# Kernel tuning notes

Measured on AMD Instinct MI355X. Metric: run time of the kernel, lower is better.

Reference implementation:

```python
import jax, jax.numpy as jnp
import numpy as np
from jax import lax

# HF MambaConfig defaults with vocab_size=2048, hidden_size=128
V, DM, NL, I, N, K, R = 2048, 128, 32, 256, 16, 4, 8  # vocab, d_model, layers, intermediate, ssm_state, conv_kernel, dt_rank
B, L = 8, 2048
EPS = 1e-5


def _rms(x, w):
    return x * lax.rsqrt(jnp.mean(x * x, axis=-1, keepdims=True) + EPS) * w


def _block(x, p):
    res = x
    h = _rms(x, p['norm_w'])
    hz = h @ p['in_proj_w'].T                            # (B,L,2I)
    hs, gate = hz[..., :I], hz[..., I:]
    # depthwise causal conv over time
    c = lax.conv_general_dilated(hs.transpose(0, 2, 1), p['conv_w'][:, None, :],
                                 (1,), [(K - 1, 0)],
                                 dimension_numbers=('NCH', 'OIH', 'NCH'),
                                 feature_group_count=I)
    hs = jax.nn.silu((c + p['conv_b'][None, :, None]).transpose(0, 2, 1))  # (B,L,I)
    xp = hs @ p['x_proj_w'].T                            # (B,L,R+2N)
    dt, Bm, Cm = xp[..., :R], xp[..., R:R + N], xp[..., R + N:]
    dt = jax.nn.softplus(dt @ p['dt_proj_w'].T + p['dt_proj_b'])           # (B,L,I)
    A = -jnp.exp(p['A_log'])                             # (I,N)
    dA = jnp.exp(dt[..., None] * A)                      # (B,L,I,N)
    dBu = dt[..., None] * Bm[:, :, None, :] * hs[..., None]               # (B,L,I,N)

    # selective scan: h_t = dA_t * h_{t-1} + dBu_t, via parallel associative scan
    def comb(e1, e2):
        a1, b1 = e1
        a2, b2 = e2
        return a2 * a1, a2 * b1 + b2

    _, hstates = lax.associative_scan(comb, (dA, dBu), axis=1)
    y = jnp.einsum('blin,bln->bli', hstates, Cm) + hs * p['D']
    y = y * jax.nn.silu(gate)
    return res + y @ p['out_proj_w'].T


def setup_inputs() -> dict:
    key = jax.random.key(0)
    ks = jax.random.split(key, 10)

    def rn(k, shape, s):
        return jax.random.normal(k, shape, jnp.float32) * s

    a_init = jnp.tile(jnp.log(jnp.arange(1, N + 1, dtype=jnp.float32)), (NL, I, 1))
    return {
        'x': jax.random.randint(ks[0], (B, L), 0, V),
        'embed': rn(ks[1], (V, DM), 0.02),
        'in_proj_w': rn(ks[2], (NL, 2 * I, DM), DM ** -0.5),
        'conv_w': rn(ks[3], (NL, I, K), K ** -0.5),
        'conv_b': jnp.zeros((NL, I), jnp.float32),
        'x_proj_w': rn(ks[4], (NL, R + 2 * N, I), I ** -0.5),
        'dt_proj_w': rn(ks[5], (NL, I, R), R ** -0.5),
        'dt_proj_b': jnp.full((NL, I), float(np.log(np.expm1(0.01))), jnp.float32),
        'A_log': a_init,
        'D': jnp.ones((NL, I), jnp.float32),
        'out_proj_w': rn(ks[6], (NL, DM, I), I ** -0.5),
        'norm_w': jnp.ones((NL, DM), jnp.float32),
        'norm_f_w': jnp.ones((DM,), jnp.float32),
        'head_w': rn(ks[7], (V, DM), 0.02),
        'head_b': jnp.zeros((V,), jnp.float32),
    }


def reference(x, embed, in_proj_w, conv_w, conv_b, x_proj_w, dt_proj_w, dt_proj_b,
              A_log, D, out_proj_w, norm_w, norm_f_w, head_w, head_b):
    h = embed[x]                                          # (B,L,DM)
    layer_params = {'in_proj_w': in_proj_w, 'conv_w': conv_w, 'conv_b': conv_b,
                    'x_proj_w': x_proj_w, 'dt_proj_w': dt_proj_w, 'dt_proj_b': dt_proj_b,
                    'A_log': A_log, 'D': D, 'out_proj_w': out_proj_w, 'norm_w': norm_w}
    h, _ = lax.scan(lambda c, p: (_block(c, p), None), h, layer_params)
    h = _rms(h, norm_f_w)
    return h @ head_w.T + head_b                          # (B,L,V) logits
```

## Files before the change

kernel.cpp:

```cpp
#include <hip/hip_runtime.h>
#include <hip/hip_bf16.h>

#define LSEQ 2048
#define NCH 64
#define CHL 32

typedef __attribute__((ext_vector_type(8))) short bf16x8;
typedef __attribute__((ext_vector_type(4))) float f32x4;
typedef __hip_bfloat16 bf16;

__device__ __forceinline__ void gload_lds16(const void* g, void* l) {
  __builtin_amdgcn_global_load_lds(
      (const __attribute__((address_space(1))) void*)g,
      (__attribute__((address_space(3))) void*)l, 16, 0, 0);
}

__device__ __forceinline__ void split_bf16(float v, bf16& h, bf16& l) {
  h = __float2bfloat16(v);
  l = __float2bfloat16(v - __bfloat162float(h));
}

__global__ __launch_bounds__(256) void embed_kernel(const int* __restrict__ x,
                                                    const float* __restrict__ emb,
                                                    float* __restrict__ h) {
  int idx = blockIdx.x * 256 + threadIdx.x;
  int t = idx >> 7;
  int d = idx & 127;
  h[idx] = emb[(size_t)x[t] * 128 + d];
}

__global__ __launch_bounds__(256) void cast_split_kernel(const float* __restrict__ src,
                                                         bf16* __restrict__ hi,
                                                         bf16* __restrict__ lo, int n) {
  int i = blockIdx.x * 256 + threadIdx.x;
  if (i < n) { bf16 h, l; split_bf16(src[i], h, l); hi[i] = h; lo[i] = l; }
}

__global__ __launch_bounds__(256) void cast_xproj_kernel(const float* __restrict__ src,
                                                         bf16* __restrict__ hi,
                                                         bf16* __restrict__ lo) {
  int i = blockIdx.x * 256 + threadIdx.x;
  int k = i & 255, n = (i >> 8) & 63, l = i >> 14;
  float v = (n < 40) ? src[((size_t)l * 40 + n) * 256 + k] : 0.f;
  bf16 h, lw; split_bf16(v, h, lw);
  hi[i] = h; lo[i] = lw;
}

__global__ __launch_bounds__(256) void rmsnorm_split_kernel(const float* __restrict__ hin,
                                                            const float* __restrict__ w,
                                                            bf16* __restrict__ hout_h,
                                                            bf16* __restrict__ hout_l) {
  int row = blockIdx.x * 4 + (threadIdx.x >> 6);
  int lane = threadIdx.x & 63;
  float2 v = *(const float2*)&hin[(size_t)row * 128 + lane * 2];
  float ss = v.x * v.x + v.y * v.y;
  #pragma unroll
  for (int m = 1; m < 64; m <<= 1) ss += __shfl_xor(ss, m);
  float rstd = rsqrtf(ss * (1.0f / 128.0f) + 1e-5f);
  float2 wv = *(const float2*)&w[lane * 2];
  float o0 = v.x * rstd * wv.x, o1 = v.y * rstd * wv.y;
  __hip_bfloat162 ph, pl;
  bf16 hh, ll;
  split_bf16(o0, hh, ll); ph.x = hh; pl.x = ll;
  split_bf16(o1, hh, ll); ph.y = hh; pl.y = ll;
  *(__hip_bfloat162*)&hout_h[(size_t)row * 128 + lane * 2] = ph;
  *(__hip_bfloat162*)&hout_l[(size_t)row * 128 + lane * 2] = pl;
}

template <int BM, int BN, int WR, int WC, int EPI>
__global__ __launch_bounds__(256) void mfma_gemm(const bf16* __restrict__ AH,
                                                 const bf16* __restrict__ AL,
                                                 const bf16* __restrict__ WH,
                                                 const bf16* __restrict__ WL,
                                                 float* __restrict__ C,
                                                 const float* __restrict__ bias,
                                                 int Nc, int Kc) {
  constexpr int WTM = BM / WR, WTN = BN / WC;
  constexpr int U = WTM / 16, V = WTN / 16;
  __shared__ bf16 AsH[BM * 64];
  __shared__ bf16 AsL[BM * 64];
  __shared__ bf16 BsH[BN * 64];
  __shared__ bf16 BsL[BN * 64];
  int tid = threadIdx.x;
  int lane = tid & 63, wid = tid >> 6;
  int wr = wid / WC, wc = wid % WC;
  int row0 = blockIdx.x * BM, col0 = blockIdx.y * BN;
  int l15 = lane & 15, l4 = lane >> 4;
  f32x4 acc[U][V] = {};
  for (int k0 = 0; k0 < Kc; k0 += 64) {
    __syncthreads();
    #pragma unroll
    for (int it = 0; it < BM / 32; ++it) {
      int chunk = it * 256 + tid;
      int r = chunk >> 3;
      int clog = (chunk & 7) ^ (r & 7);
      size_t goff = (size_t)(row0 + r) * Kc + k0 + clog * 8;
      gload_lds16(AH + goff, &AsH[chunk * 8]);
      gload_lds16(AL + goff, &AsL[chunk * 8]);
    }
    #pragma unroll
    for (int it = 0; it < BN / 32; ++it) {
      int chunk = it * 256 + tid;
      int r = chunk >> 3;
      int clog = (chunk & 7) ^ (r & 7);
      size_t goff = (size_t)(col0 + r) * Kc + k0 + clog * 8;
      gload_lds16(WH + goff, &BsH[chunk * 8]);
      gload_lds16(WL + goff, &BsL[chunk * 8]);
    }
    __syncthreads();
    #pragma unroll
    for (int kk = 0; kk < 2; ++kk) {
      bf16x8 afh[U], afl[U], bfh[V], bfl[V];
      #pragma unroll
      for (int u = 0; u < U; ++u) {
        int r = wr * WTM + u * 16 + l15;
        int csw = (kk * 4 + l4) ^ (r & 7);
        afh[u] = *(const bf16x8*)&AsH[r * 64 + csw * 8];
        afl[u] = *(const bf16x8*)&AsL[r * 64 + csw * 8];
      }
      #pragma unroll
      for (int v = 0; v < V; ++v) {
        int r = wc * WTN + v * 16 + l15;
        int csw = (kk * 4 + l4) ^ (r & 7);
        bfh[v] = *(const bf16x8*)&BsH[r * 64 + csw * 8];
        bfl[v] = *(const bf16x8*)&BsL[r * 64 + csw * 8];
      }
      #pragma unroll
      for (int u = 0; u < U; ++u)
        #pragma unroll
        for (int v = 0; v < V; ++v) {
          acc[u][v] = __builtin_amdgcn_mfma_f32_16x16x32_bf16(afh[u], bfh[v], acc[u][v], 0, 0, 0);
          acc[u][v] = __builtin_amdgcn_mfma_f32_16x16x32_bf16(afl[u], bfh[v], acc[u][v], 0, 0, 0);
          acc[u][v] = __builtin_amdgcn_mfma_f32_16x16x32_bf16(afh[u], bfl[v], acc[u][v], 0, 0, 0);
        }
    }
  }
  #pragma unroll
  for (int u = 0; u < U; ++u) {
    int rbase = row0 + wr * WTM + u * 16 + l4 * 4;
    #pragma unroll
    for (int v = 0; v < V; ++v) {
      int col = col0 + wc * WTN + v * 16 + l15;
      #pragma unroll
      for (int q = 0; q < 4; ++q) {
        size_t off = (size_t)(rbase + q) * Nc + col;
        float val = acc[u][v][q];
        if (EPI == 2) val += bias[col];
        C[off] = val;
      }
    }
  }
}

__global__ __launch_bounds__(256) void inproj_kernel(const bf16* __restrict__ AH,
                                                     const bf16* __restrict__ AL,
                                                     const bf16* __restrict__ WH,
                                                     const bf16* __restrict__ WL,
                                                     float* __restrict__ hzx,
                                                     float* __restrict__ gate_f) {
  constexpr int BM = 128, BN = 128;
  __shared__ bf16 AsH[BM * 64];
  __shared__ bf16 AsL[BM * 64];
  __shared__ bf16 BsH[BN * 64];
  __shared__ bf16 BsL[BN * 64];
  int tid = threadIdx.x;
  int lane = tid & 63, wid = tid >> 6;
  int wr = wid >> 1, wc = wid & 1;
  int row0 = blockIdx.x * BM, col0 = blockIdx.y * BN;
  int l15 = lane & 15, l4 = lane >> 4;
  f32x4 acc[4][4] = {};
  for (int k0 = 0; k0 < 128; k0 += 64) {
    __syncthreads();
    #pragma unroll
    for (int it = 0; it < 4; ++it) {
      int chunk = it * 256 + tid;
      int r = chunk >> 3;
      int clog = (chunk & 7) ^ (r & 7);
      size_t goff = (size_t)(row0 + r) * 128 + k0 + clog * 8;
      gload_lds16(AH + goff, &AsH[chunk * 8]);
      gload_lds16(AL + goff, &AsL[chunk * 8]);
      size_t woff = (size_t)(col0 + r) * 128 + k0 + clog * 8;
      gload_lds16(WH + woff, &BsH[chunk * 8]);
      gload_lds16(WL + woff, &BsL[chunk * 8]);
    }
    __syncthreads();
    #pragma unroll
    for (int kk = 0; kk < 2; ++kk) {
      bf16x8 afh[4], afl[4], bfh[4], bfl[4];
      #pragma unroll
      for (int u = 0; u < 4; ++u) {
        int r = wr * 64 + u * 16 + l15;
        int csw = (kk * 4 + l4) ^ (r & 7);
        afh[u] = *(const bf16x8*)&AsH[r * 64 + csw * 8];
        afl[u] = *(const bf16x8*)&AsL[r * 64 + csw * 8];
      }
      #pragma unroll
      for (int v = 0; v < 4; ++v) {
        int r = wc * 64 + v * 16 + l15;
        int csw = (kk * 4 + l4) ^ (r & 7);
        bfh[v] = *(const bf16x8*)&BsH[r * 64 + csw * 8];
        bfl[v] = *(const bf16x8*)&BsL[r * 64 + csw * 8];
      }
      #pragma unroll
      for (int u = 0; u < 4; ++u)
        #pragma unroll
        for (int v = 0; v < 4; ++v) {
          acc[u][v] = __builtin_amdgcn_mfma_f32_16x16x32_bf16(afh[u], bfh[v], acc[u][v], 0, 0, 0);
          acc[u][v] = __builtin_amdgcn_mfma_f32_16x16x32_bf16(afl[u], bfh[v], acc[u][v], 0, 0, 0);
          acc[u][v] = __builtin_amdgcn_mfma_f32_16x16x32_bf16(afh[u], bfl[v], acc[u][v], 0, 0, 0);
        }
    }
  }
  bool isgate = (col0 >= 256);
  #pragma unroll
  for (int u = 0; u < 4; ++u) {
    int rbase = row0 + wr * 64 + u * 16 + l4 * 4;
    #pragma unroll
    for (int v = 0; v < 4; ++v) {
      int col = col0 + wc * 64 + v * 16 + l15;
      #pragma unroll
      for (int q = 0; q < 4; ++q) {
        float val = acc[u][v][q];
        if (!isgate) {
          hzx[(size_t)(rbase + q) * 256 + col] = val;
        } else {
          float s = val / (1.0f + __expf(-val));
          gate_f[(size_t)(rbase + q) * 256 + (col - 256)] = s;
        }
      }
    }
  }
}

__global__ __launch_bounds__(256) void xproj_scan_kernel(const float* __restrict__ hzx,
                                                         const float* __restrict__ cw,
                                                         const float* __restrict__ cb,
                                                         const bf16* __restrict__ WH,
                                                         const bf16* __restrict__ WL,
                                                         const float* __restrict__ Wdt,
                                                         const float* __restrict__ bdt,
                                                         const float* __restrict__ A_log,
                                                         __hip_bfloat162* __restrict__ hs_p,
                                                         float* __restrict__ xp,
                                                         float* __restrict__ dtb,
                                                         float* __restrict__ Pb,
                                                         float* __restrict__ Sb) {
  __shared__ bf16 AsH[32 * 64];
  __shared__ bf16 AsL[32 * 64];
  __shared__ bf16 BsH[64 * 64];
  __shared__ bf16 BsL[64 * 64];
  __shared__ float xq[32][24];
  __shared__ __hip_bfloat162 hs_lds[32][257];
  int tid = threadIdx.x;
  int lane = tid & 63, wid = tid >> 6;
  int wr = wid >> 1, wc = wid & 1;
  int row0 = blockIdx.x * 32;
  int l15 = lane & 15, l4 = lane >> 4;
  int r = tid >> 3, cslot = tid & 7;
  int tok = row0 + r;
  int lpos = tok & (LSEQ - 1);
  f32x4 acc[1][2] = {};
  for (int k0 = 0; k0 < 256; k0 += 64) {
    __syncthreads();
    {
      int kb = k0 + ((cslot ^ (r & 7)) << 3);
      const float* hp = &hzx[(size_t)tok * 256 + kb];
      float x3[8], x2[8], x1[8], x0[8];
      *(float4*)&x3[0] = *(const float4*)(hp);
      *(float4*)&x3[4] = *(const float4*)(hp + 4);
      if (lpos >= 1) { *(float4*)&x2[0] = *(const float4*)(hp - 256); *(float4*)&x2[4] = *(const float4*)(hp - 252); }
      else { *(float4*)&x2[0] = make_float4(0,0,0,0); *(float4*)&x2[4] = make_float4(0,0,0,0); }
      if (lpos >= 2) { *(float4*)&x1[0] = *(const float4*)(hp - 512); *(float4*)&x1[4] = *(const float4*)(hp - 508); }
      else { *(float4*)&x1[0] = make_float4(0,0,0,0); *(float4*)&x1[4] = make_float4(0,0,0,0); }
      if (lpos >= 3) { *(float4*)&x0[0] = *(const float4*)(hp - 768); *(float4*)&x0[4] = *(const float4*)(hp - 764); }
      else { *(float4*)&x0[0] = make_float4(0,0,0,0); *(float4*)&x0[4] = make_float4(0,0,0,0); }
      bf16 tH[8], tL[8];
      __hip_bfloat162 pk[8];
      #pragma unroll
      for (int j = 0; j < 8; ++j) {
        float4 w = *(const float4*)&cw[(kb + j) * 4];
        float s = cb[kb + j];
        s = fmaf(x0[j], w.x, s);
        s = fmaf(x1[j], w.y, s);
        s = fmaf(x2[j], w.z, s);
        s = fmaf(x3[j], w.w, s);
        s = s / (1.0f + __expf(-s));
        split_bf16(s, tH[j], tL[j]);
        pk[j].x = tH[j]; pk[j].y = tL[j];
        hs_lds[r][kb + j] = pk[j];
      }
      *(bf16x8*)&AsH[tid * 8] = *(const bf16x8*)tH;
      *(bf16x8*)&AsL[tid * 8] = *(const bf16x8*)tL;
      *(float4*)&hs_p[(size_t)tok * 256 + kb]     = *(const float4*)&pk[0];
      *(float4*)&hs_p[(size_t)tok * 256 + kb + 4] = *(const float4*)&pk[4];
    }
    #pragma unroll
    for (int it = 0; it < 2; ++it) {
      int chunk = it * 256 + tid;
      int rr = chunk >> 3;
      int clog = (chunk & 7) ^ (rr & 7);
      size_t goff = (size_t)rr * 256 + k0 + clog * 8;
      gload_lds16(WH + goff, &BsH[chunk * 8]);
      gload_lds16(WL + goff, &BsL[chunk * 8]);
    }
    __syncthreads();
    #pragma unroll
    for (int kk = 0; kk < 2; ++kk) {
      bf16x8 afh, afl, bfh[2], bfl[2];
      {
        int rr = wr * 16 + l15;
        int csw = (kk * 4 + l4) ^ (rr & 7);
        afh = *(const bf16x8*)&AsH[rr * 64 + csw * 8];
        afl = *(const bf16x8*)&AsL[rr * 64 + csw * 8];
      }
      #pragma unroll
      for (int v = 0; v < 2; ++v) {
        int rr = wc * 32 + v * 16 + l15;
        int csw = (kk * 4 + l4) ^ (rr & 7);
        bfh[v] = *(const bf16x8*)&BsH[rr * 64 + csw * 8];
        bfl[v] = *(const bf16x8*)&BsL[rr * 64 + csw * 8];
      }
      #pragma unroll
      for (int v = 0; v < 2; ++v) {
        acc[0][v] = __builtin_amdgcn_mfma_f32_16x16x32_bf16(afh, bfh[v], acc[0][v], 0, 0, 0);
        acc[0][v] = __builtin_amdgcn_mfma_f32_16x16x32_bf16(afl, bfh[v], acc[0][v], 0, 0, 0);
        acc[0][v] = __builtin_amdgcn_mfma_f32_16x16x32_bf16(afh, bfl[v], acc[0][v], 0, 0, 0);
      }
    }
  }
  {
    int rbase = wr * 16 + l4 * 4;
    #pragma unroll
    for (int v = 0; v < 2; ++v) {
      int col = wc * 32 + v * 16 + l15;
      #pragma unroll
      for (int q = 0; q < 4; ++q) {
        float val = acc[0][v][q];
        xp[(size_t)(row0 + rbase + q) * 64 + col] = val;
        if (col < 24) xq[rbase + q][col] = val;
      }
    }
  }
  __syncthreads();
  {
    int i = tid;
    float A[16];
    {
      const float4* ap = (const float4*)&A_log[i * 16];
      #pragma unroll
      for (int q = 0; q < 4; ++q) {
        float4 a = ap[q];
        A[q * 4 + 0] = -__expf(a.x); A[q * 4 + 1] = -__expf(a.y);
        A[q * 4 + 2] = -__expf(a.z); A[q * 4 + 3] = -__expf(a.w);
      }
    }
    const float* wr8 = Wdt + i * 8;
    float w0 = wr8[0], w1 = wr8[1], w2 = wr8[2], w3 = wr8[3];
    float w4 = wr8[4], w5 = wr8[5], w6 = wr8[6], w7 = wr8[7];
    float bv = bdt[i];
    float P[16], S[16];
    #pragma unroll
    for (int n = 0; n < 16; ++n) { P[n] = 1.0f; S[n] = 0.0f; }
    for (int tt = 0; tt < 32; ++tt) {
      const float* q = xq[tt];
      float s = bv;
      s = fmaf(q[0], w0, s); s = fmaf(q[1], w1, s);
      s = fmaf(q[2], w2, s); s = fmaf(q[3], w3, s);
      s = fmaf(q[4], w4, s); s = fmaf(q[5], w5, s);
      s = fmaf(q[6], w6, s); s = fmaf(q[7], w7, s);
      float dtv = (s > 20.0f) ? s : log1pf(__expf(s));
      dtb[(size_t)(row0 + tt) * 256 + i] = dtv;
      __hip_bfloat162 hp = hs_lds[tt][i];
      float hsv = __bfloat162float(hp.x) + __bfloat162float(hp.y);
      float dh = dtv * hsv;
      #pragma unroll
      for (int n = 0; n < 16; ++n) {
        float e = __expf(dtv * A[n]);
        P[n] *= e;
        S[n] = fmaf(S[n], e, dh * q[8 + n]);
      }
    }
    size_t base = ((size_t)blockIdx.x << 12) + i * 16;
    #pragma unroll
    for (int qq = 0; qq < 4; ++qq) {
      *(float4*)&Pb[base + qq * 4] = make_float4(P[qq * 4], P[qq * 4 + 1], P[qq * 4 + 2], P[qq * 4 + 3]);
      *(float4*)&Sb[base + qq * 4] = make_float4(S[qq * 4], S[qq * 4 + 1], S[qq * 4 + 2], S[qq * 4 + 3]);
    }
  }
}

__global__ __launch_bounds__(256) void outproj_norm_kernel(const bf16* __restrict__ AH,
                                                           const bf16* __restrict__ AL,
                                                           const bf16* __restrict__ WH,
                                                           const bf16* __restrict__ WL,
                                                           const float* __restrict__ nw,
                                                           float* __restrict__ Ch,
                                                           bf16* __restrict__ hn_h,
                                                           bf16* __restrict__ hn_l) {
  constexpr int BM = 32, BN = 128;
  __shared__ bf16 AsH[BM * 64];
  __shared__ bf16 AsL[BM * 64];
  __shared__ bf16 BsH[BN * 64];
  __shared__ bf16 BsL[BN * 64];
  __shared__ float ssq[32][2];
  int tid = threadIdx.x;
  int lane = tid & 63, wid = tid >> 6;
  int wr = wid >> 1, wc = wid & 1;
  int row0 = blockIdx.x * BM;
  int l15 = lane & 15, l4 = lane >> 4;
  f32x4 acc[1][4] = {};
  for (int k0 = 0; k0 < 256; k0 += 64) {
    __syncthreads();
    {
      int chunk = tid;
      int r = chunk >> 3;
      int clog = (chunk & 7) ^ (r & 7);
      size_t goff = (size_t)(row0 + r) * 256 + k0 + clog * 8;
      gload_lds16(AH + goff, &AsH[chunk * 8]);
      gload_lds16(AL + goff, &AsL[chunk * 8]);
    }
    #pragma unroll
    for (int it = 0; it < 4; ++it) {
      int chunk = it * 256 + tid;
      int r = chunk >> 3;
      int clog = (chunk & 7) ^ (r & 7);
      size_t goff = (size_t)r * 256 + k0 + clog * 8;
      gload_lds16(WH + goff, &BsH[chunk * 8]);
      gload_lds16(WL + goff, &BsL[chunk * 8]);
    }
    __syncthreads();
    #pragma unroll
    for (int kk = 0; kk < 2; ++kk) {
      bf16x8 afh, afl, bfh[4], bfl[4];
      {
        int r = wr * 16 + l15;
        int csw = (kk * 4 + l4) ^ (r & 7);
        afh = *(const bf16x8*)&AsH[r * 64 + csw * 8];
        afl = *(const bf16x8*)&AsL[r * 64 + csw * 8];
      }
      #pragma unroll
      for (int v = 0; v < 4; ++v) {
        int r = wc * 64 + v * 16 + l15;
        int csw = (kk * 4 + l4) ^ (r & 7);
        bfh[v] = *(const bf16x8*)&BsH[r * 64 + csw * 8];
        bfl[v] = *(const bf16x8*)&BsL[r * 64 + csw * 8];
      }
      #pragma unroll
      for (int v = 0; v < 4; ++v) {
        acc[0][v] = __builtin_amdgcn_mfma_f32_16x16x32_bf16(afh, bfh[v], acc[0][v], 0, 0, 0);
        acc[0][v] = __builtin_amdgcn_mfma_f32_16x16x32_bf16(afl, bfh[v], acc[0][v], 0, 0, 0);
        acc[0][v] = __builtin_amdgcn_mfma_f32_16x16x32_bf16(afh, bfl[v], acc[0][v], 0, 0, 0);
      }
    }
  }
  int rloc = wr * 16 + l4 * 4;
  float vals[4][4];
  #pragma unroll
  for (int v = 0; v < 4; ++v) {
    int col = wc * 64 + v * 16 + l15;
    #pragma unroll
    for (int q = 0; q < 4; ++q) {
      size_t off = (size_t)(row0 + rloc + q) * 128 + col;
      float val = acc[0][v][q] + Ch[off];
      vals[q][v] = val;
      Ch[off] = val;
    }
  }
  #pragma unroll
  for (int q = 0; q < 4; ++q) {
    float ss = vals[q][0] * vals[q][0] + vals[q][1] * vals[q][1]
             + vals[q][2] * vals[q][2] + vals[q][3] * vals[q][3];
    ss += __shfl_xor(ss, 1, 16);
    ss += __shfl_xor(ss, 2, 16);
    ss += __shfl_xor(ss, 4, 16);
    ss += __shfl_xor(ss, 8, 16);
    if (l15 == 0) ssq[rloc + q][wc] = ss;
  }
  __syncthreads();
  #pragma unroll
  for (int q = 0; q < 4; ++q) {
    float rstd = rsqrtf((ssq[rloc + q][0] + ssq[rloc + q][1]) * (1.0f / 128.0f) + 1e-5f);
    #pragma unroll
    for (int v = 0; v < 4; ++v) {
      int col = wc * 64 + v * 16 + l15;
      float o = vals[q][v] * rstd * nw[col];
      bf16 hh, ll;
      split_bf16(o, hh, ll);
      size_t off = (size_t)(row0 + rloc + q) * 128 + col;
      hn_h[off] = hh;
      hn_l[off] = ll;
    }
  }
}

__global__ __launch_bounds__(256) void scanB_kernel(const float* __restrict__ Pb,
                                                    const float* __restrict__ Sb,
                                                    float* __restrict__ Ib) {
  int g = blockIdx.x * 256 + threadIdx.x;
  int b = g >> 12, rem = g & 4095;
  float s = 0.0f;
  for (int cc = 0; cc < NCH; ++cc) {
    size_t off = ((size_t)(b * NCH + cc) << 12) + rem;
    Ib[off] = s;
    s = fmaf(s, Pb[off], Sb[off]);
  }
}

__global__ __launch_bounds__(256) void scanC_kernel(const float* __restrict__ dtb,
                                                    const __hip_bfloat162* __restrict__ hs_p,
                                                    const float* __restrict__ xp,
                                                    const float* __restrict__ A_log,
                                                    const float* __restrict__ Dp,
                                                    const float* __restrict__ gate_f,
                                                    const float* __restrict__ Ib,
                                                    bf16* __restrict__ y_h,
                                                    bf16* __restrict__ y_l) {
  int b = blockIdx.x, c = blockIdx.y, i = threadIdx.x;
  float A[16];
  {
    const float4* ap = (const float4*)&A_log[i * 16];
    #pragma unroll
    for (int q = 0; q < 4; ++q) {
      float4 a = ap[q];
      A[q * 4 + 0] = -__expf(a.x); A[q * 4 + 1] = -__expf(a.y);
      A[q * 4 + 2] = -__expf(a.z); A[q * 4 + 3] = -__expf(a.w);
    }
  }
  float st[16];
  {
    size_t base = ((size_t)(b * NCH + c) << 12) + i * 16;
    #pragma unroll
    for (int q = 0; q < 4; ++q) {
      float4 s4 = *(const float4*)&Ib[base + q * 4];
      st[q * 4 + 0] = s4.x; st[q * 4 + 1] = s4.y; st[q * 4 + 2] = s4.z; st[q * 4 + 3] = s4.w;
    }
  }
  float Dv = Dp[i];
  int t0 = b * LSEQ + c * CHL;
  for (int l = 0; l < CHL; ++l) {
    size_t t = t0 + l;
    float dtv = dtb[t * 256 + i];
    __hip_bfloat162 hp = hs_p[t * 256 + i];
    float hsv = __bfloat162float(hp.x) + __bfloat162float(hp.y);
    float dh = dtv * hsv;
    float Bv[16], Cv[16];
    #pragma unroll
    for (int q = 0; q < 4; ++q) {
      float4 bv = *(const float4*)&xp[t * 64 + 8 + q * 4];
      Bv[q * 4 + 0] = bv.x; Bv[q * 4 + 1] = bv.y; Bv[q * 4 + 2] = bv.z; Bv[q * 4 + 3] = bv.w;
      float4 cv = *(const float4*)&xp[t * 64 + 24 + q * 4];
      Cv[q * 4 + 0] = cv.x; Cv[q * 4 + 1] = cv.y; Cv[q * 4 + 2] = cv.z; Cv[q * 4 + 3] = cv.w;
    }
    float y0 = 0.f, y1 = 0.f, y2 = 0.f, y3 = 0.f;
    #pragma unroll
    for (int q = 0; q < 4; ++q) {
      float e0 = __expf(dtv * A[q * 4 + 0]);
      float e1 = __expf(dtv * A[q * 4 + 1]);
      float e2 = __expf(dtv * A[q * 4 + 2]);
      float e3 = __expf(dtv * A[q * 4 + 3]);
      st[q * 4 + 0] = fmaf(st[q * 4 + 0], e0, dh * Bv[q * 4 + 0]);
      st[q * 4 + 1] = fmaf(st[q * 4 + 1], e1, dh * Bv[q * 4 + 1]);
      st[q * 4 + 2] = fmaf(st[q * 4 + 2], e2, dh * Bv[q * 4 + 2]);
      st[q * 4 + 3] = fmaf(st[q * 4 + 3], e3, dh * Bv[q * 4 + 3]);
      y0 = fmaf(st[q * 4 + 0], Cv[q * 4 + 0], y0);
      y1 = fmaf(st[q * 4 + 1], Cv[q * 4 + 1], y1);
      y2 = fmaf(st[q * 4 + 2], Cv[q * 4 + 2], y2);
      y3 = fmaf(st[q * 4 + 3], Cv[q * 4 + 3], y3);
    }
    float y = ((y0 + y1) + (y2 + y3)) + hsv * Dv;
    float g = gate_f[t * 256 + i];
    float val = y * g;
    bf16 hh, ll;
    split_bf16(val, hh, ll);
    y_h[t * 256 + i] = hh;
    y_l[t * 256 + i] = ll;
  }
}

extern "C" void kernel_launch(void* const* d_in, const int* in_sizes, int n_in,
                              void* d_out, int out_size, void* d_ws, size_t ws_size,
                              hipStream_t stream) {
  const int* x           = (const int*)d_in[0];
  const float* embed     = (const float*)d_in[1];
  const float* in_proj_w = (const float*)d_in[2];
  const float* conv_w    = (const float*)d_in[3];
  const float* conv_b    = (const float*)d_in[4];
  const float* x_proj_w  = (const float*)d_in[5];
  const float* dt_proj_w = (const float*)d_in[6];
  const float* dt_proj_b = (const float*)d_in[7];
  const float* A_log     = (const float*)d_in[8];
  const float* Dp        = (const float*)d_in[9];
  const float* out_proj_w= (const float*)d_in[10];
  const float* norm_w    = (const float*)d_in[11];
  const float* norm_f_w  = (const float*)d_in[12];
  const float* head_w    = (const float*)d_in[13];
  const float* head_b    = (const float*)d_in[14];

  float* out = (float*)d_out;
  float* ws  = (float*)d_ws;

  float* hzx     = out;
  float* gate_f  = out + 4194304;
  __hip_bfloat162* hs_p = (__hip_bfloat162*)(out + 8388608);
  float* dtb     = out + 12582912;
  float* xp      = out + 16777216;
  float* Pb      = out + 17825792;
  float* Sb      = out + 19922944;
  bf16*  y_h     = (bf16*)(out + 17825792);
  bf16*  y_l     = (bf16*)(out + 19922944);
  float* h       = out + 22020096;
  bf16*  w_in_h  = (bf16*)(out + 24117248);
  bf16*  w_in_l  = (bf16*)(out + 25165824);
  bf16*  w_x_h   = (bf16*)(out + 26214400);
  bf16*  w_x_l   = (bf16*)(out + 26476544);
  bf16*  w_out_h = (bf16*)(out + 26738688);
  bf16*  w_out_l = (bf16*)(out + 27262976);
  float* Ib      = out + 27787264;

  bf16* hn_h     = (bf16*)ws;
  bf16* hn_l     = (bf16*)(ws + 1048576);
  bf16* w_head_h = (bf16*)(ws + 2097152);
  bf16* w_head_l = (bf16*)(ws + 2228224);

  cast_split_kernel<<<8192, 256, 0, stream>>>(in_proj_w, w_in_h, w_in_l, 2097152);
  cast_xproj_kernel<<<2048, 256, 0, stream>>>(x_proj_w, w_x_h, w_x_l);
  cast_split_kernel<<<4096, 256, 0, stream>>>(out_proj_w, w_out_h, w_out_l, 1048576);
  cast_split_kernel<<<1024, 256, 0, stream>>>(head_w, w_head_h, w_head_l, 262144);

  embed_kernel<<<8192, 256, 0, stream>>>(x, embed, h);
  rmsnorm_split_kernel<<<4096, 256, 0, stream>>>(h, norm_w, hn_h, hn_l);

  for (int l = 0; l < 32; ++l) {
    inproj_kernel<<<dim3(128, 4), 256, 0, stream>>>(
        hn_h, hn_l, w_in_h + (size_t)l * 512 * 128, w_in_l + (size_t)l * 512 * 128,
        hzx, gate_f);
    xproj_scan_kernel<<<512, 256, 0, stream>>>(
        hzx, conv_w + l * 1024, conv_b + l * 256,
        w_x_h + (size_t)l * 64 * 256, w_x_l + (size_t)l * 64 * 256,
        dt_proj_w + l * 2048, dt_proj_b + l * 256, A_log + l * 4096,
        hs_p, xp, dtb, Pb, Sb);
    scanB_kernel<<<128, 256, 0, stream>>>(Pb, Sb, Ib);
    scanC_kernel<<<dim3(8, NCH), 256, 0, stream>>>(
        dtb, hs_p, xp, A_log + l * 4096, Dp + l * 256, gate_f, Ib, y_h, y_l);
    const float* nwnext = (l < 31) ? (norm_w + (l + 1) * 128) : norm_f_w;
    outproj_norm_kernel<<<512, 256, 0, stream>>>(
        y_h, y_l, w_out_h + (size_t)l * 128 * 256, w_out_l + (size_t)l * 128 * 256,
        nwnext, h, hn_h, hn_l);
  }

  mfma_gemm<128, 128, 2, 2, 2><<<dim3(128, 16), 256, 0, stream>>>(
      hn_h, hn_l, w_head_h, w_head_l, out, head_b, 2048, 128);
}
```

Baseline: 3.316 ms.

## Fuse scan output phase into out_proj GEMM with RMSNorm via LDS

Merges the per-chunk scan output kernel (scanC) into the out_proj+norm kernel. Each block first replays its 32-timestep chunk of the selective scan and writes the gated y values as packed hi/lo bf16 into LDS, then feeds them to the MFMA GEMM instead of loading them from global memory. This drops one launch per layer and the global write/read of y_h/y_l. In exchange it uses more LDS per block (an extra 32x257 bf16x2 buffer), which may lower occupancy, and the repacking from LDS is done with scalar reads.

```diff
diff --git a/kernel.cpp b/kernel.cpp
--- a/kernel.cpp
+++ b/kernel.cpp
@@ -389,110 +389,6 @@
   }
 }
 
-__global__ __launch_bounds__(256) void outproj_norm_kernel(const bf16* __restrict__ AH,
-                                                           const bf16* __restrict__ AL,
-                                                           const bf16* __restrict__ WH,
-                                                           const bf16* __restrict__ WL,
-                                                           const float* __restrict__ nw,
-                                                           float* __restrict__ Ch,
-                                                           bf16* __restrict__ hn_h,
-                                                           bf16* __restrict__ hn_l) {
-  constexpr int BM = 32, BN = 128;
-  __shared__ bf16 AsH[BM * 64];
-  __shared__ bf16 AsL[BM * 64];
-  __shared__ bf16 BsH[BN * 64];
-  __shared__ bf16 BsL[BN * 64];
-  __shared__ float ssq[32][2];
-  int tid = threadIdx.x;
-  int lane = tid & 63, wid = tid >> 6;
-  int wr = wid >> 1, wc = wid & 1;
-  int row0 = blockIdx.x * BM;
-  int l15 = lane & 15, l4 = lane >> 4;
-  f32x4 acc[1][4] = {};
-  for (int k0 = 0; k0 < 256; k0 += 64) {
-    __syncthreads();
-    {
-      int chunk = tid;
-      int r = chunk >> 3;
-      int clog = (chunk & 7) ^ (r & 7);
-      size_t goff = (size_t)(row0 + r) * 256 + k0 + clog * 8;
-      gload_lds16(AH + goff, &AsH[chunk * 8]);
-      gload_lds16(AL + goff, &AsL[chunk * 8]);
-    }
-    #pragma unroll
-    for (int it = 0; it < 4; ++it) {
-      int chunk = it * 256 + tid;
-      int r = chunk >> 3;
-      int clog = (chunk & 7) ^ (r & 7);
-      size_t goff = (size_t)r * 256 + k0 + clog * 8;
-      gload_lds16(WH + goff, &BsH[chunk * 8]);
-      gload_lds16(WL + goff, &BsL[chunk * 8]);
-    }
-    __syncthreads();
-    #pragma unroll
-    for (int kk = 0; kk < 2; ++kk) {
-      bf16x8 afh, afl, bfh[4], bfl[4];
-      {
-        int r = wr * 16 + l15;
-        int csw = (kk * 4 + l4) ^ (r & 7);
-        afh = *(const bf16x8*)&AsH[r * 64 + csw * 8];
-        afl = *(const bf16x8*)&AsL[r * 64 + csw * 8];
-      }
-      #pragma unroll
-      for (int v = 0; v < 4; ++v) {
-        int r = wc * 64 + v * 16 + l15;
-        int csw = (kk * 4 + l4) ^ (r & 7);
-        bfh[v] = *(const bf16x8*)&BsH[r * 64 + csw * 8];
-        bfl[v] = *(const bf16x8*)&BsL[r * 64 + csw * 8];
-      }
-      #pragma unroll
-      for (int v = 0; v < 4; ++v) {
-        acc[0][v] = __builtin_amdgcn_mfma_f32_16x16x32_bf16(afh, bfh[v], acc[0][v], 0, 0, 0);
-        acc[0][v] = __builtin_amdgcn_mfma_f32_16x16x32_bf16(afl, bfh[v], acc[0][v], 0, 0, 0);
-        acc[0][v] = __builtin_amdgcn_mfma_f32_16x16x32_bf16(afh, bfl[v], acc[0][v], 0, 0, 0);
-      }
-    }
-  }
-  int rloc = wr * 16 + l4 * 4;
-  float vals[4][4];
-  #pragma unroll
-  for (int v = 0; v < 4; ++v) {
-    int col = wc * 64 + v * 16 + l15;
-    #pragma unroll
-    for (int q = 0; q < 4; ++q) {
-      size_t off = (size_t)(row0 + rloc + q) * 128 + col;
-      float val = acc[0][v][q] + Ch[off];
-      vals[q][v] = val;
-      Ch[off] = val;
-    }
-  }
-  #pragma unroll
-  for (int q = 0; q < 4; ++q) {
-    float ss = vals[q][0] * vals[q][0] + vals[q][1] * vals[q][1]
-             + vals[q][2] * vals[q][2] + vals[q][3] * vals[q][3];
-    ss += __shfl_xor(ss, 1, 16);
-    ss += __shfl_xor(ss, 2, 16);
-    ss += __shfl_xor(ss, 4, 16);
-    ss += __shfl_xor(ss, 8, 16);
-    if (l15 == 0) ssq[rloc + q][wc] = ss;
-  }
-  __syncthreads();
-  #pragma unroll
-  for (int q = 0; q < 4; ++q) {
-    float rstd = rsqrtf((ssq[rloc + q][0] + ssq[rloc + q][1]) * (1.0f / 128.0f) + 1e-5f);
-    #pragma unroll
-    for (int v = 0; v < 4; ++v) {
-      int col = wc * 64 + v * 16 + l15;
-      float o = vals[q][v] * rstd * nw[col];
-      bf16 hh, ll;
-      split_bf16(o, hh, ll);
-      size_t off = (size_t)(row0 + rloc + q) * 128 + col;
-      hn_h[off] = hh;
-      hn_l[off] = ll;
-    }
-  }
-}
-
 __global__ __launch_bounds__(256) void scanB_kernel(const float* __restrict__ Pb,
                                                     const float* __restrict__ Sb,
                                                     float* __restrict__ Ib) {
@@ -506,74 +402,178 @@
   }
 }
 
-__global__ __launch_bounds__(256) void scanC_kernel(const float* __restrict__ dtb,
-                                                    const __hip_bfloat162* __restrict__ hs_p,
-                                                    const float* __restrict__ xp,
-                                                    const float* __restrict__ A_log,
-                                                    const float* __restrict__ Dp,
-                                                    const float* __restrict__ gate_f,
-                                                    const float* __restrict__ Ib,
-                                                    bf16* __restrict__ y_h,
-                                                    bf16* __restrict__ y_l) {
-  int b = blockIdx.x, c = blockIdx.y, i = threadIdx.x;
-  float A[16];
+__global__ __launch_bounds__(256) void outproj_scan_norm_kernel(const float* __restrict__ dtb,
+                                                                const __hip_bfloat162* __restrict__ hs_p,
+                                                                const float* __restrict__ xp,
+                                                                const float* __restrict__ A_log,
+                                                                const float* __restrict__ Dp,
+                                                                const float* __restrict__ gate_f,
+                                                                const float* __restrict__ Ib,
+                                                                const bf16* __restrict__ WH,
+                                                                const bf16* __restrict__ WL,
+                                                                const float* __restrict__ nw,
+                                                                float* __restrict__ Ch,
+                                                                bf16* __restrict__ hn_h,
+                                                                bf16* __restrict__ hn_l) {
+  __shared__ bf16 AsH[32 * 64];
+  __shared__ bf16 AsL[32 * 64];
+  __shared__ bf16 BsH[128 * 64];
+  __shared__ bf16 BsL[128 * 64];
+  __shared__ __hip_bfloat162 y_lds[32][257];
+  __shared__ float ssq[32][2];
+  int tid = threadIdx.x;
+  int lane = tid & 63, wid = tid >> 6;
+  int wr = wid >> 1, wc = wid & 1;
+  int row0 = blockIdx.x * 32;
+  int l15 = lane & 15, l4 = lane >> 4;
   {
-    const float4* ap = (const float4*)&A_log[i * 16];
+    int i = tid;
+    float A[16];
+    {
+      const float4* ap = (const float4*)&A_log[i * 16];
+      #pragma unroll
+      for (int q = 0; q < 4; ++q) {
+        float4 a = ap[q];
+        A[q * 4 + 0] = -__expf(a.x); A[q * 4 + 1] = -__expf(a.y);
+        A[q * 4 + 2] = -__expf(a.z); A[q * 4 + 3] = -__expf(a.w);
+      }
+    }
+    float st[16];
+    {
+      size_t base = ((size_t)blockIdx.x << 12) + i * 16;
+      #pragma unroll
+      for (int q = 0; q < 4; ++q) {
+        float4 s4 = *(const float4*)&Ib[base + q * 4];
+        st[q * 4 + 0] = s4.x; st[q * 4 + 1] = s4.y; st[q * 4 + 2] = s4.z; st[q * 4 + 3] = s4.w;
+      }
+    }
+    float Dv = Dp[i];
+    for (int tt = 0; tt < 32; ++tt) {
+      size_t t = row0 + tt;
+      float dtv = dtb[t * 256 + i];
+      __hip_bfloat162 hp = hs_p[t * 256 + i];
+      float hsv = __bfloat162float(hp.x) + __bfloat162float(hp.y);
+      float dh = dtv * hsv;
+      float Bv[16], Cv[16];
+      #pragma unroll
+      for (int q = 0; q < 4; ++q) {
+        float4 bv = *(const float4*)&xp[t * 64 + 8 + q * 4];
+        Bv[q * 4 + 0] = bv.x; Bv[q * 4 + 1] = bv.y; Bv[q * 4 + 2] = bv.z; Bv[q * 4 + 3] = bv.w;
+        float4 cv = *(const float4*)&xp[t * 64 + 24 + q * 4];
+        Cv[q * 4 + 0] = cv.x; Cv[q * 4 + 1] = cv.y; Cv[q * 4 + 2] = cv.z; Cv[q * 4 + 3] = cv.w;
+      }
+      float y0 = 0.f, y1 = 0.f, y2 = 0.f, y3 = 0.f;
+      #pragma unroll
+      for (int q = 0; q < 4; ++q) {
+        float e0 = __expf(dtv * A[q * 4 + 0]);
+        float e1 = __expf(dtv * A[q * 4 + 1]);
+        float e2 = __expf(dtv * A[q * 4 + 2]);
+        float e3 = __expf(dtv * A[q * 4 + 3]);
+        st[q * 4 + 0] = fmaf(st[q * 4 + 0], e0, dh * Bv[q * 4 + 0]);
+        st[q * 4 + 1] = fmaf(st[q * 4 + 1], e1, dh * Bv[q * 4 + 1]);
+        st[q * 4 + 2] = fmaf(st[q * 4 + 2], e2, dh * Bv[q * 4 + 2]);
+        st[q * 4 + 3] = fmaf(st[q * 4 + 3], e3, dh * Bv[q * 4 + 3]);
+        y0 = fmaf(st[q * 4 + 0], Cv[q * 4 + 0], y0);
+        y1 = fmaf(st[q * 4 + 1], Cv[q * 4 + 1], y1);
+        y2 = fmaf(st[q * 4 + 2], Cv[q * 4 + 2], y2);
+        y3 = fmaf(st[q * 4 + 3], Cv[q * 4 + 3], y3);
+      }
+      float y = ((y0 + y1) + (y2 + y3)) + hsv * Dv;
+      float g = gate_f[t * 256 + i];
+      float val = y * g;
+      bf16 hh, ll;
+      split_bf16(val, hh, ll);
+      __hip_bfloat162 pk; pk.x = hh; pk.y = ll;
+      y_lds[tt][i] = pk;
+    }
+  }
+  f32x4 acc[1][4] = {};
+  for (int k0 = 0; k0 < 256; k0 += 64) {
+    __syncthreads();
+    {
+      int chunk = tid;
+      int r = chunk >> 3;
+      int kb = k0 + (((chunk & 7) ^ (r & 7)) << 3);
+      bf16 tH[8], tL[8];
+      #pragma unroll
+      for (int j = 0; j < 8; ++j) {
+        __hip_bfloat162 pk = y_lds[r][kb + j];
+        tH[j] = pk.x; tL[j] = pk.y;
+      }
+      *(bf16x8*)&AsH[tid * 8] = *(const bf16x8*)tH;
+      *(bf16x8*)&AsL[tid * 8] = *(const bf16x8*)tL;
+    }
+    #pragma unroll
+    for (int it = 0; it < 4; ++it) {
+      int chunk = it * 256 + tid;
+      int r = chunk >> 3;
+      int clog = (chunk & 7) ^ (r & 7);
+      size_t goff = (size_t)r * 256 + k0 + clog * 8;
+      gload_lds16(WH + goff, &BsH[chunk * 8]);
+      gload_lds16(WL + goff, &BsL[chunk * 8]);
+    }
+    __syncthreads();
+    #pragma unroll
+    for (int kk = 0; kk < 2; ++kk) {
+      bf16x8 afh, afl, bfh[4], bfl[4];
+      {
+        int r = wr * 16 + l15;
+        int csw = (kk * 4 + l4) ^ (r & 7);
+        afh = *(const bf16x8*)&AsH[r * 64 + csw * 8];
+        afl = *(const bf16x8*)&AsL[r * 64 + csw * 8];
+      }
+      #pragma unroll
+      for (int v = 0; v < 4; ++v) {
+        int r = wc * 64 + v * 16 + l15;
+        int csw = (kk * 4 + l4) ^ (r & 7);
+        bfh[v] = *(const bf16x8*)&BsH[r * 64 + csw * 8];
+        bfl[v] = *(const bf16x8*)&BsL[r * 64 + csw * 8];
+      }
+      #pragma unroll
+      for (int v = 0; v < 4; ++v) {
+        acc[0][v] = __builtin_amdgcn_mfma_f32_16x16x32_bf16(afh, bfh[v], acc[0][v], 0, 0, 0);
+        acc[0][v] = __builtin_amdgcn_mfma_f32_16x16x32_bf16(afl, bfh[v], acc[0][v], 0, 0, 0);
+        acc[0][v] = __builtin_amdgcn_mfma_f32_16x16x32_bf16(afh, bfl[v], acc[0][v], 0, 0, 0);
+      }
+    }
+  }
+  int rloc = wr * 16 + l4 * 4;
+  float vals[4][4];
+  #pragma unroll
+  for (int v = 0; v < 4; ++v) {
+    int col = wc * 64 + v * 16 + l15;
     #pragma unroll
     for (int q = 0; q < 4; ++q) {
-      float4 a = ap[q];
-      A[q * 4 + 0] = -__expf(a.x); A[q * 4 + 1] = -__expf(a.y);
-      A[q * 4 + 2] = -__expf(a.z); A[q * 4 + 3] = -__expf(a.w);
-    }
-  }
-  float st[16];
-  {
-    size_t base = ((size_t)(b * NCH + c) << 12) + i * 16;
-    #pragma unroll
-    for (int q = 0; q < 4; ++q) {
-      float4 s4 = *(const float4*)&Ib[base + q * 4];
-      st[q * 4 + 0] = s4.x; st[q * 4 + 1] = s4.y; st[q * 4 + 2] = s4.z; st[q * 4 + 3] = s4.w;
-    }
-  }
-  float Dv = Dp[i];
-  int t0 = b * LSEQ + c * CHL;
-  for (int l = 0; l < CHL; ++l) {
-    size_t t = t0 + l;
-    float dtv = dtb[t * 256 + i];
-    __hip_bfloat162 hp = hs_p[t * 256 + i];
-    float hsv = __bfloat162float(hp.x) + __bfloat162float(hp.y);
-    float dh = dtv * hsv;
-    float Bv[16], Cv[16];
-    #pragma unroll
-    for (int q = 0; q < 4; ++q) {
-      float4 bv = *(const float4*)&xp[t * 64 + 8 + q * 4];
-      Bv[q * 4 + 0] = bv.x; Bv[q * 4 + 1] = bv.y; Bv[q * 4 + 2] = bv.z; Bv[q * 4 + 3] = bv.w;
-      float4 cv = *(const float4*)&xp[t * 64 + 24 + q * 4];
-      Cv[q * 4 + 0] = cv.x; Cv[q * 4 + 1] = cv.y; Cv[q * 4 + 2] = cv.z; Cv[q * 4 + 3] = cv.w;
-    }
-    float y0 = 0.f, y1 = 0.f, y2 = 0.f, y3 = 0.f;
-    #pragma unroll
-    for (int q = 0; q < 4; ++q) {
-      float e0 = __expf(dtv * A[q * 4 + 0]);
-      float e1 = __expf(dtv * A[q * 4 + 1]);
-      float e2 = __expf(dtv * A[q * 4 + 2]);
-      float e3 = __expf(dtv * A[q * 4 + 3]);
-      st[q * 4 + 0] = fmaf(st[q * 4 + 0], e0, dh * Bv[q * 4 + 0]);
-      st[q * 4 + 1] = fmaf(st[q * 4 + 1], e1, dh * Bv[q * 4 + 1]);
-      st[q * 4 + 2] = fmaf(st[q * 4 + 2], e2, dh * Bv[q * 4 + 2]);
-      st[q * 4 + 3] = fmaf(st[q * 4 + 3], e3, dh * Bv[q * 4 + 3]);
-      y0 = fmaf(st[q * 4 + 0], Cv[q * 4 + 0], y0);
-      y1 = fmaf(st[q * 4 + 1], Cv[q * 4 + 1], y1);
-      y2 = fmaf(st[q * 4 + 2], Cv[q * 4 + 2], y2);
-      y3 = fmaf(st[q * 4 + 3], Cv[q * 4 + 3], y3);
-    }
-    float y = ((y0 + y1) + (y2 + y3)) + hsv * Dv;
-    float g = gate_f[t * 256 + i];
-    float val = y * g;
-    bf16 hh, ll;
-    split_bf16(val, hh, ll);
-    y_h[t * 256 + i] = hh;
-    y_l[t * 256 + i] = ll;
+      size_t off = (size_t)(row0 + rloc + q) * 128 + col;
+      float val = acc[0][v][q] + Ch[off];
+      vals[q][v] = val;
+      Ch[off] = val;
+    }
+  }
+  #pragma unroll
+  for (int q = 0; q < 4; ++q) {
+    float ss = vals[q][0] * vals[q][0] + vals[q][1] * vals[q][1]
+             + vals[q][2] * vals[q][2] + vals[q][3] * vals[q][3];
+    ss += __shfl_xor(ss, 1, 16);
+    ss += __shfl_xor(ss, 2, 16);
+    ss += __shfl_xor(ss, 4, 16);
+    ss += __shfl_xor(ss, 8, 16);
+    if (l15 == 0) ssq[rloc + q][wc] = ss;
+  }
+  __syncthreads();
+  #pragma unroll
+  for (int q = 0; q < 4; ++q) {
+    float rstd = rsqrtf((ssq[rloc + q][0] + ssq[rloc + q][1]) * (1.0f / 128.0f) + 1e-5f);
+    #pragma unroll
+    for (int v = 0; v < 4; ++v) {
+      int col = wc * 64 + v * 16 + l15;
+      float o = vals[q][v] * rstd * nw[col];
+      bf16 hh, ll;
+      split_bf16(o, hh, ll);
+      size_t off = (size_t)(row0 + rloc + q) * 128 + col;
+      hn_h[off] = hh;
+      hn_l[off] = ll;
+    }
   }
 }
 
@@ -606,8 +606,6 @@
   float* xp      = out + 16777216;
   float* Pb      = out + 17825792;
   float* Sb      = out + 19922944;
-  bf16*  y_h     = (bf16*)(out + 17825792);
-  bf16*  y_l     = (bf16*)(out + 19922944);
   float* h       = out + 22020096;
   bf16*  w_in_h  = (bf16*)(out + 24117248);
   bf16*  w_in_l  = (bf16*)(out + 25165824);
@@ -640,11 +638,10 @@
         dt_proj_w + l * 2048, dt_proj_b + l * 256, A_log + l * 4096,
         hs_p, xp, dtb, Pb, Sb);
     scanB_kernel<<<128, 256, 0, stream>>>(Pb, Sb, Ib);
-    scanC_kernel<<<dim3(8, NCH), 256, 0, stream>>>(
-        dtb, hs_p, xp, A_log + l * 4096, Dp + l * 256, gate_f, Ib, y_h, y_l);
     const float* nwnext = (l < 31) ? (norm_w + (l + 1) * 128) : norm_f_w;
-    outproj_norm_kernel<<<512, 256, 0, stream>>>(
-        y_h, y_l, w_out_h + (size_t)l * 128 * 256, w_out_l + (size_t)l * 128 * 256,
+    outproj_scan_norm_kernel<<<512, 256, 0, stream>>>(
+        dtb, hs_p, xp, A_log + l * 4096, Dp + l * 256, gate_f, Ib,
+        w_out_h + (size_t)l * 128 * 256, w_out_l + (size_t)l * 128 * 256,
         nwnext, h, hn_h, hn_l);
   }
 
```

Measured after the change: 3.130 ms (median of 3 runs). 1.06x faster.
